# Optimization experiments

Measured on AMD Instinct MI355X. Metric: run time of the kernel, lower is better.

Reference implementation:

```python
import jax, jax.numpy as jnp
import numpy as np

NUM_EXPERTS = 8
TOP_K = 2


def setup_inputs() -> dict:
    key = jax.random.key(0)
    ks = jax.random.split(key, 5)
    B, S, D, F, E = 4, 2048, 1024, 4096, NUM_EXPERTS
    scale = 0.02
    x = jax.random.normal(ks[0], (B, S, D), dtype=jnp.float32)
    W_gate = jax.random.normal(ks[1], (E, D), dtype=jnp.float32) * scale  # router: logits = x @ W_gate.T
    Wg = jax.random.normal(ks[2], (E, F, D), dtype=jnp.float32) * scale   # per-expert gate_proj
    Wu = jax.random.normal(ks[3], (E, F, D), dtype=jnp.float32) * scale   # per-expert up_proj
    Wd = jax.random.normal(ks[4], (E, D, F), dtype=jnp.float32) * scale   # per-expert down_proj
    return {"x": x, "W_gate": W_gate, "Wg": Wg, "Wu": Wu, "Wd": Wd}


def reference(x, W_gate, Wg, Wu, Wd):
    # Router: softmax over experts, then top-k, renormalize.
    gate_logits = jnp.einsum('bsd,ed->bse', x, W_gate)
    probs = jax.nn.softmax(gate_logits, axis=-1)
    top_w, top_i = jax.lax.top_k(probs, TOP_K)                # (B,S,K)
    top_w = top_w / jnp.sum(top_w, axis=-1, keepdims=True)

    output = jnp.zeros_like(x)
    for e in range(NUM_EXPERTS):
        # combined routing weight for expert e (0 for tokens not routed to e)
        w_e = jnp.sum(jnp.where(top_i == e, top_w, 0.0), axis=-1)  # (B,S)
        gate = jax.nn.silu(jnp.einsum('bsd,fd->bsf', x, Wg[e]))
        up = jnp.einsum('bsd,fd->bsf', x, Wu[e])
        out_e = jnp.einsum('bsf,df->bsd', gate * up, Wd[e])
        output = output + out_e * w_e[..., None]
    return output
```

## Files before the change

### kernel.cpp

```cpp
#include <hip/hip_runtime.h>
#include <hip/hip_bf16.h>

#define T_TOK 8192
#define D_DIM 1024
#define F_DIM 4096
#define NE 8

#define BM 128
#define BK 32

#define BM2 256
#define BN2 128
#define BK2 64
#define KT2 (D_DIM / BK2)

typedef _Float16 v8h __attribute__((ext_vector_type(8)));
typedef float f32x4 __attribute__((ext_vector_type(4)));

__device__ __forceinline__ void async_lds16(void* lds, const void* g) {
    __builtin_amdgcn_global_load_lds(
        (const __attribute__((address_space(1))) void*)g,
        (__attribute__((address_space(3))) void*)lds,
        16, 0, 0);
}

template<int OFF>
__device__ __forceinline__ v8h ds128(unsigned a) {
    v8h r;
    asm volatile("ds_read_b128 %0, %1 offset:%2" : "=v"(r) : "v"(a), "n"(OFF));
    return r;
}

#define LGKM0 asm volatile("s_waitcnt lgkmcnt(0)" ::: "memory")
#define VMCNT0 asm volatile("s_waitcnt vmcnt(0)" ::: "memory")
#define SB0 __builtin_amdgcn_sched_barrier(0)

__global__ void router_kernel(const float* __restrict__ x,
                              const float* __restrict__ Wgate,
                              int* __restrict__ cnt,
                              int* __restrict__ rows,
                              float* __restrict__ wts) {
    int t = blockIdx.x;
    int lane = threadIdx.x;
    const float* xr = x + (size_t)t * D_DIM;
    float acc[NE];
#pragma unroll
    for (int e = 0; e < NE; ++e) acc[e] = 0.f;
#pragma unroll
    for (int i = 0; i < D_DIM / 64; ++i) {
        int d = i * 64 + lane;
        float xv = xr[d];
#pragma unroll
        for (int e = 0; e < NE; ++e) acc[e] += xv * Wgate[e * D_DIM + d];
    }
#pragma unroll
    for (int off = 32; off > 0; off >>= 1) {
#pragma unroll
        for (int e = 0; e < NE; ++e) acc[e] += __shfl_xor(acc[e], off, 64);
    }
    if (lane == 0) {
        int e0 = 0;
#pragma unroll
        for (int e = 1; e < NE; ++e) if (acc[e] > acc[e0]) e0 = e;
        int e1 = (e0 == 0) ? 1 : 0;
#pragma unroll
        for (int e = 0; e < NE; ++e) if (e != e0 && acc[e] > acc[e1]) e1 = e;
        float w0 = 1.f / (1.f + __expf(acc[e1] - acc[e0]));
        float w1 = 1.f - w0;
        int p0 = atomicAdd(&cnt[e0], 1);
        rows[e0 * T_TOK + p0] = 2 * t;
        wts[e0 * T_TOK + p0] = w0;
        int p1 = atomicAdd(&cnt[e1], 1);
        rows[e1 * T_TOK + p1] = 2 * t + 1;
        wts[e1 * T_TOK + p1] = w1;
    }
}

__global__ void f32to16_kernel(const float* __restrict__ src, _Float16* __restrict__ dst) {
    int i = blockIdx.x * blockDim.x + threadIdx.x;
    float4 v = ((const float4*)src)[i];
    union { _Float16 h[4]; uint2 u; } pk;
    pk.h[0] = (_Float16)v.x; pk.h[1] = (_Float16)v.y;
    pk.h[2] = (_Float16)v.z; pk.h[3] = (_Float16)v.w;
    *(uint2*)&dst[(size_t)i * 4] = pk.u;
}

__global__ __launch_bounds__(512, 2)
void gateup_kernel(const _Float16* __restrict__ Xh,
                   const _Float16* __restrict__ Wgh,
                   const _Float16* __restrict__ Wuh,
                   const int* __restrict__ cnt,
                   const int* __restrict__ rows,
                   const float* __restrict__ wts,
                   _Float16* __restrict__ H) {
    int e = blockIdx.z;
    int c = cnt[e];
    int row0 = blockIdx.y * BM2;
    if (row0 >= c) return;
    int col0 = blockIdx.x * BN2;

    __shared__ __align__(16) _Float16 Ab[2][BM2][BK2];
    __shared__ __align__(16) _Float16 Bb[2][BM2][BK2];
    __shared__ int hrow_s[BM2];
    __shared__ float w_s[BM2];

    int tid = threadIdx.x;
    int lane = tid & 63;
    int wv = tid >> 6;
    int wr = wv >> 2;
    int wc = wv & 3;

    if (tid < BM2) {
        int p = row0 + tid;
        if (p < c) { hrow_s[tid] = rows[e * T_TOK + p]; w_s[tid] = wts[e * T_TOK + p]; }
        else       { hrow_s[tid] = -1;                  w_s[tid] = 0.f; }
    }
    __syncthreads();

    int l8 = lane >> 3;
    int g  = lane & 7;
    int lg = g ^ l8;

    int r0 = wv * 16 + l8;
    int r1 = r0 + 8;

    int hA00 = hrow_s[r0],       hA01 = hrow_s[r1];
    int hA10 = hrow_s[128 + r0], hA11 = hrow_s[128 + r1];
    const _Float16* sA00 = Xh + (size_t)(hA00 >= 0 ? (hA00 >> 1) : 0) * D_DIM + lg * 8;
    const _Float16* sA01 = Xh + (size_t)(hA01 >= 0 ? (hA01 >> 1) : 0) * D_DIM + lg * 8;
    const _Float16* sA10 = Xh + (size_t)(hA10 >= 0 ? (hA10 >> 1) : 0) * D_DIM + lg * 8;
    const _Float16* sA11 = Xh + (size_t)(hA11 >= 0 ? (hA11 >> 1) : 0) * D_DIM + lg * 8;
    const _Float16* sB00 = Wgh + ((size_t)e * F_DIM + col0 + r0) * D_DIM + lg * 8;
    const _Float16* sB01 = Wgh + ((size_t)e * F_DIM + col0 + r1) * D_DIM + lg * 8;
    const _Float16* sB10 = Wuh + ((size_t)e * F_DIM + col0 + r0) * D_DIM + lg * 8;
    const _Float16* sB11 = Wuh + ((size_t)e * F_DIM + col0 + r1) * D_DIM + lg * 8;

    int stO0 = wv * 2048 + lane * 16;

    int m16 = lane & 15, q4 = lane >> 4;
    int rx = m16 & 7;
    int cb0 = ((q4 ^ rx) << 4);
    int cb1 = (((4 + q4) ^ rx) << 4);

    unsigned Abase = (unsigned)(size_t)(__attribute__((address_space(3))) void*)&Ab[0][0][0]
                     + (unsigned)((wr * 16 + m16) * 128);
    unsigned Bbase = (unsigned)(size_t)(__attribute__((address_space(3))) void*)&Bb[0][0][0]
                     + (unsigned)(m16 * 128 + wc * 4096);
    unsigned A0 = Abase + cb0, A1 = Abase + cb1;
    unsigned B0 = Bbase + cb0, B1 = Bbase + cb1;

    {
        char* a0 = (char*)Ab + stO0;
        char* b0 = (char*)Bb + stO0;
        async_lds16(b0,                sB00);
        async_lds16(b0 + 1024,         sB01);
        async_lds16(a0,                sA00);
        async_lds16(a0 + 1024,         sA01);
        async_lds16(b0 + 16384,        sB10);
        async_lds16(b0 + 16384 + 1024, sB11);
        async_lds16(a0 + 16384,        sA10);
        async_lds16(a0 + 16384 + 1024, sA11);
    }

    f32x4 accg[8][2], accu[8][2];
#pragma unroll
    for (int i = 0; i < 8; ++i)
#pragma unroll
        for (int j = 0; j < 2; ++j) { accg[i][j] = (f32x4)0.f; accu[i][j] = (f32x4)0.f; }

    int cur = 0;
#pragma unroll 1
    for (int t = 0; t < KT2; ++t) {
        int kn = (t + 1 < KT2) ? (t + 1) * BK2 : 0;
        int nb = cur ^ 1;

        VMCNT0;
        __builtin_amdgcn_s_barrier();
        SB0;

        {
            char* aD = (char*)Ab + nb * 32768 + stO0;
            char* bD = (char*)Bb + nb * 32768 + stO0;
            async_lds16(bD,                sB00 + kn);
            async_lds16(bD + 1024,         sB01 + kn);
            async_lds16(aD,                sA00 + kn);
            async_lds16(aD + 1024,         sA01 + kn);
            async_lds16(bD + 16384,        sB10 + kn);
            async_lds16(bD + 16384 + 1024, sB11 + kn);
            async_lds16(aD + 16384,        sA10 + kn);
            async_lds16(aD + 16384 + 1024, sA11 + kn);
        }
        SB0;

        unsigned cOff = (unsigned)(cur * 32768);
        unsigned a0 = A0 + cOff, a1 = A1 + cOff;
        unsigned b0 = B0 + cOff, b1 = B1 + cOff;

        v8h af[4][2], bg[2][2], bu[2][2];

        af[0][0] = ds128<0>(a0);      af[0][1] = ds128<0>(a1);
        af[1][0] = ds128<4096>(a0);   af[1][1] = ds128<4096>(a1);
        af[2][0] = ds128<8192>(a0);   af[2][1] = ds128<8192>(a1);
        af[3][0] = ds128<12288>(a0);  af[3][1] = ds128<12288>(a1);
        bg[0][0] = ds128<0>(b0);      bg[0][1] = ds128<0>(b1);
        bg[1][0] = ds128<2048>(b0);   bg[1][1] = ds128<2048>(b1);
        bu[0][0] = ds128<16384>(b0);  bu[0][1] = ds128<16384>(b1);
        bu[1][0] = ds128<18432>(b0);  bu[1][1] = ds128<18432>(b1);
        LGKM0;
        SB0;

        __builtin_amdgcn_s_setprio(1);
#pragma unroll
        for (int i = 0; i < 4; ++i)
#pragma unroll
            for (int j = 0; j < 2; ++j) {
                accg[i][j] = __builtin_amdgcn_mfma_f32_16x16x32_f16(af[i][0], bg[j][0], accg[i][j], 0, 0, 0);
                accg[i][j] = __builtin_amdgcn_mfma_f32_16x16x32_f16(af[i][1], bg[j][1], accg[i][j], 0, 0, 0);
            }
#pragma unroll
        for (int i = 0; i < 4; ++i)
#pragma unroll
            for (int j = 0; j < 2; ++j) {
                accu[i][j] = __builtin_amdgcn_mfma_f32_16x16x32_f16(af[i][0], bu[j][0], accu[i][j], 0, 0, 0);
                accu[i][j] = __builtin_amdgcn_mfma_f32_16x16x32_f16(af[i][1], bu[j][1], accu[i][j], 0, 0, 0);
            }
        __builtin_amdgcn_s_setprio(0);
        SB0;

        af[0][0] = ds128<16384>(a0);  af[0][1] = ds128<16384>(a1);
        af[1][0] = ds128<20480>(a0);  af[1][1] = ds128<20480>(a1);
        af[2][0] = ds128<24576>(a0);  af[2][1] = ds128<24576>(a1);
        af[3][0] = ds128<28672>(a0);  af[3][1] = ds128<28672>(a1);
        LGKM0;
        SB0;

        __builtin_amdgcn_s_setprio(1);
#pragma unroll
        for (int i = 0; i < 4; ++i)
#pragma unroll
            for (int j = 0; j < 2; ++j) {
                accg[i + 4][j] = __builtin_amdgcn_mfma_f32_16x16x32_f16(af[i][0], bg[j][0], accg[i + 4][j], 0, 0, 0);
                accg[i + 4][j] = __builtin_amdgcn_mfma_f32_16x16x32_f16(af[i][1], bg[j][1], accg[i + 4][j], 0, 0, 0);
            }
#pragma unroll
        for (int i = 0; i < 4; ++i)
#pragma unroll
            for (int j = 0; j < 2; ++j) {
                accu[i + 4][j] = __builtin_amdgcn_mfma_f32_16x16x32_f16(af[i][0], bu[j][0], accu[i + 4][j], 0, 0, 0);
                accu[i + 4][j] = __builtin_amdgcn_mfma_f32_16x16x32_f16(af[i][1], bu[j][1], accu[i + 4][j], 0, 0, 0);
            }
        __builtin_amdgcn_s_setprio(0);

        cur = nb;
    }

    int cl = lane & 15;
#pragma unroll
    for (int i = 0; i < 8; ++i) {
#pragma unroll
        for (int j = 0; j < 2; ++j) {
            f32x4 gv = accg[i][j];
            f32x4 uv = accu[i][j];
#pragma unroll
            for (int r4 = 0; r4 < 4; ++r4) {
                int r = i * 32 + wr * 16 + q4 * 4 + r4;
                int hr = hrow_s[r];
                if (hr < 0) continue;
                float gg = gv[r4];
                float h = gg / (1.f + __expf(-gg)) * w_s[r] * uv[r4];
                H[(size_t)hr * F_DIM + col0 + (wc * 2 + j) * 16 + cl] = (_Float16)h;
            }
        }
    }
}

__global__ __launch_bounds__(256, 2)
void down_kernel(const _Float16* __restrict__ H,
                 const _Float16* __restrict__ Wdh,
                 const int* __restrict__ cnt,
                 const int* __restrict__ rows,
                 float* __restrict__ O) {
    int e = blockIdx.z;
    int c = cnt[e];
    int row0 = blockIdx.y * BM;
    if (row0 >= c) return;
    int col0 = blockIdx.x * 128;

    __shared__ __align__(16) _Float16 As[BM][BK];
    __shared__ __align__(16) _Float16 Bs[128][BK];
    __shared__ int hrow_s[BM];

    int tid = threadIdx.x;
    int lane = tid & 63;
    int wave = tid >> 6;
    int wr = wave >> 1, wc = wave & 1;

    if (tid < BM) {
        int p = row0 + tid;
        hrow_s[tid] = (p < c) ? rows[e * T_TOK + p] : -1;
    }
    __syncthreads();

    int srow = tid >> 2;
    int kch = tid & 3;
    int hr0 = hrow_s[srow], hr1 = hrow_s[srow + 64];
    int r0 = (hr0 >= 0) ? hr0 : 0;
    int r1 = (hr1 >= 0) ? hr1 : 0;

    const _Float16* a0 = H + (size_t)r0 * F_DIM + kch * 8;
    const _Float16* a1 = H + (size_t)r1 * F_DIM + kch * 8;
    const _Float16* b0 = Wdh + ((size_t)e * D_DIM + col0 + srow) * F_DIM + kch * 8;
    const _Float16* b1 = b0 + (size_t)64 * F_DIM;

    _Float16* lA0 = &As[srow][kch * 8];
    _Float16* lA1 = &As[srow + 64][kch * 8];
    _Float16* lB0 = &Bs[srow][kch * 8];
    _Float16* lB1 = &Bs[srow + 64][kch * 8];

    f32x4 acc[4][4];
#pragma unroll
    for (int i = 0; i < 4; ++i)
#pragma unroll
        for (int j = 0; j < 4; ++j) acc[i][j] = (f32x4)0.f;

    int m16 = lane & 15, q8 = (lane >> 4) * 8;

    for (int k0 = 0; k0 < F_DIM; k0 += BK) {
        async_lds16(lA0, a0 + k0);
        async_lds16(lA1, a1 + k0);
        async_lds16(lB0, b0 + k0);
        async_lds16(lB1, b1 + k0);
        __syncthreads();

        v8h af[4], bf[4];
#pragma unroll
        for (int i = 0; i < 4; ++i)
            af[i] = *(const v8h*)&As[wr * 64 + i * 16 + m16][q8];
#pragma unroll
        for (int j = 0; j < 4; ++j)
            bf[j] = *(const v8h*)&Bs[wc * 64 + j * 16 + m16][q8];
#pragma unroll
        for (int i = 0; i < 4; ++i)
#pragma unroll
            for (int j = 0; j < 4; ++j)
                acc[i][j] = __builtin_amdgcn_mfma_f32_16x16x32_f16(af[i], bf[j], acc[i][j], 0, 0, 0);
        __syncthreads();
    }

    int q = lane >> 4, cl = lane & 15;
#pragma unroll
    for (int i = 0; i < 4; ++i) {
#pragma unroll
        for (int r4 = 0; r4 < 4; ++r4) {
            int r = wr * 64 + i * 16 + q * 4 + r4;
            int hr = hrow_s[r];
            if (hr < 0) continue;
#pragma unroll
            for (int j = 0; j < 4; ++j) {
                int col = col0 + wc * 64 + j * 16 + cl;
                O[(size_t)hr * D_DIM + col] = acc[i][j][r4];
            }
        }
    }
}

__global__ void combine_kernel(const float* __restrict__ O, float* __restrict__ out) {
    int t = blockIdx.x;
    int d = threadIdx.x;
    const float4* a = (const float4*)(O + (size_t)(2 * t) * D_DIM);
    const float4* b = (const float4*)(O + (size_t)(2 * t + 1) * D_DIM);
    float4 va = a[d], vb = b[d];
    float4 r; r.x = va.x + vb.x; r.y = va.y + vb.y; r.z = va.z + vb.z; r.w = va.w + vb.w;
    ((float4*)(out + (size_t)t * D_DIM))[d] = r;
}

extern "C" void kernel_launch(void* const* d_in, const int* in_sizes, int n_in,
                              void* d_out, int out_size, void* d_ws, size_t ws_size,
                              hipStream_t stream) {
    const float* x     = (const float*)d_in[0];
    const float* Wgate = (const float*)d_in[1];
    const float* Wg    = (const float*)d_in[2];
    const float* Wu    = (const float*)d_in[3];
    const float* Wd    = (const float*)d_in[4];
    float* out = (float*)d_out;

    char* w = (char*)d_ws;
    int*      cnt  = (int*)w;
    int*      rows = (int*)(w + 1024);
    float*    wts  = (float*)(w + 263168);
    _Float16* Xh   = (_Float16*)(w + 525312);

    const size_t OFF_WGH = 17302528;
    const size_t OFF_WUH = 84411392;
    const size_t OFF_WDH = 151520256;
    const size_t OFF_H   = 218629120;
    const size_t OFF_O   = 352846848;

    _Float16* Wgh = (_Float16*)(w + OFF_WGH);
    _Float16* Wuh = (_Float16*)(w + OFF_WUH);
    _Float16* Wdh = (_Float16*)(w + OFF_WDH);
    _Float16* H   = (_Float16*)(w + OFF_H);
    float*    O   = (float*)(w + OFF_O);

    hipMemsetAsync(w, 0, 1024, stream);

    router_kernel<<<T_TOK, 64, 0, stream>>>(x, Wgate, cnt, rows, wts);
    f32to16_kernel<<<(T_TOK * D_DIM / 4) / 256, 256, 0, stream>>>(x, Xh);

    const int WN4 = (NE * F_DIM * D_DIM / 4);
    f32to16_kernel<<<WN4 / 256, 256, 0, stream>>>(Wg, Wgh);
    f32to16_kernel<<<WN4 / 256, 256, 0, stream>>>(Wu, Wuh);
    f32to16_kernel<<<WN4 / 256, 256, 0, stream>>>(Wd, Wdh);

    gateup_kernel<<<dim3(F_DIM / BN2, T_TOK / BM2, NE), 512, 0, stream>>>(
        Xh, Wgh, Wuh, cnt, rows, wts, H);
    down_kernel<<<dim3(D_DIM / 128, T_TOK / BM, NE), 256, 0, stream>>>(
        H, Wdh, cnt, rows, O);
    combine_kernel<<<T_TOK, 256, 0, stream>>>(O, out);
}
```

Baseline: 1.183 ms.

## Double-buffer down-projection GEMM with swizzled LDS and larger 256x128 tiles

Rewrites the down-projection kernel to use 256-row tiles with 512 threads, a BK of 64, and double-buffered LDS filled by async global-to-LDS loads so the next tile's fetch overlaps the current tile's MFMAs. LDS layout is XOR-swizzled and read with explicit ds_read_b128, and wave priority is raised around the MFMA block. The goal is to hide memory latency, cut barriers per K step, and increase reuse of the expert weight tile. Larger tiles waste more work on partially filled expert row blocks, and LDS use grows, which can limit occupancy.

```diff
diff --git a/kernel.cpp b/kernel.cpp
--- a/kernel.cpp
+++ b/kernel.cpp
@@ -6,13 +6,11 @@
 #define F_DIM 4096
 #define NE 8
 
-#define BM 128
-#define BK 32
-
 #define BM2 256
 #define BN2 128
 #define BK2 64
 #define KT2 (D_DIM / BK2)
+#define KTD (F_DIM / BK2)
 
 typedef _Float16 v8h __attribute__((ext_vector_type(8)));
 typedef float f32x4 __attribute__((ext_vector_type(4)));
@@ -274,7 +272,7 @@
     }
 }
 
-__global__ __launch_bounds__(256, 2)
+__global__ __launch_bounds__(512, 2)
 void down_kernel(const _Float16* __restrict__ H,
                  const _Float16* __restrict__ Wdh,
                  const int* __restrict__ cnt,
@@ -282,40 +280,66 @@
                  float* __restrict__ O) {
     int e = blockIdx.z;
     int c = cnt[e];
-    int row0 = blockIdx.y * BM;
+    int row0 = blockIdx.y * BM2;
     if (row0 >= c) return;
     int col0 = blockIdx.x * 128;
 
-    __shared__ __align__(16) _Float16 As[BM][BK];
-    __shared__ __align__(16) _Float16 Bs[128][BK];
-    __shared__ int hrow_s[BM];
+    __shared__ __align__(16) _Float16 Ab[2][BM2][BK2];
+    __shared__ __align__(16) _Float16 Bb[2][128][BK2];
+    __shared__ int hrow_s[BM2];
 
     int tid = threadIdx.x;
     int lane = tid & 63;
-    int wave = tid >> 6;
-    int wr = wave >> 1, wc = wave & 1;
-
-    if (tid < BM) {
+    int wv = tid >> 6;
+    int wr = wv >> 1;
+    int wc = wv & 1;
+
+    if (tid < BM2) {
         int p = row0 + tid;
         hrow_s[tid] = (p < c) ? rows[e * T_TOK + p] : -1;
     }
     __syncthreads();
 
-    int srow = tid >> 2;
-    int kch = tid & 3;
-    int hr0 = hrow_s[srow], hr1 = hrow_s[srow + 64];
-    int r0 = (hr0 >= 0) ? hr0 : 0;
-    int r1 = (hr1 >= 0) ? hr1 : 0;
-
-    const _Float16* a0 = H + (size_t)r0 * F_DIM + kch * 8;
-    const _Float16* a1 = H + (size_t)r1 * F_DIM + kch * 8;
-    const _Float16* b0 = Wdh + ((size_t)e * D_DIM + col0 + srow) * F_DIM + kch * 8;
-    const _Float16* b1 = b0 + (size_t)64 * F_DIM;
-
-    _Float16* lA0 = &As[srow][kch * 8];
-    _Float16* lA1 = &As[srow + 64][kch * 8];
-    _Float16* lB0 = &Bs[srow][kch * 8];
-    _Float16* lB1 = &Bs[srow + 64][kch * 8];
+    int l8 = lane >> 3;
+    int g  = lane & 7;
+    int lg = g ^ l8;
+
+    int r0 = wv * 16 + l8;
+    int r1 = r0 + 8;
+
+    int hA00 = hrow_s[r0],       hA01 = hrow_s[r1];
+    int hA10 = hrow_s[128 + r0], hA11 = hrow_s[128 + r1];
+    const _Float16* sA00 = H + (size_t)(hA00 >= 0 ? hA00 : 0) * F_DIM + lg * 8;
+    const _Float16* sA01 = H + (size_t)(hA01 >= 0 ? hA01 : 0) * F_DIM + lg * 8;
+    const _Float16* sA10 = H + (size_t)(hA10 >= 0 ? hA10 : 0) * F_DIM + lg * 8;
+    const _Float16* sA11 = H + (size_t)(hA11 >= 0 ? hA11 : 0) * F_DIM + lg * 8;
+    const _Float16* sB00 = Wdh + ((size_t)e * D_DIM + col0 + r0) * F_DIM + lg * 8;
+    const _Float16* sB01 = Wdh + ((size_t)e * D_DIM + col0 + r1) * F_DIM + lg * 8;
+
+    int stO0 = wv * 2048 + lane * 16;
+
+    int m16 = lane & 15, q4 = lane >> 4;
+    int rx = m16 & 7;
+    int cb0 = ((q4 ^ rx) << 4);
+    int cb1 = (((4 + q4) ^ rx) << 4);
+
+    unsigned Abase = (unsigned)(size_t)(__attribute__((address_space(3))) void*)&Ab[0][0][0]
+                     + (unsigned)((wr * 64 + m16) * 128);
+    unsigned Bbase = (unsigned)(size_t)(__attribute__((address_space(3))) void*)&Bb[0][0][0]
+                     + (unsigned)((wc * 64 + m16) * 128);
+    unsigned A0 = Abase + cb0, A1 = Abase + cb1;
+    unsigned B0 = Bbase + cb0, B1 = Bbase + cb1;
+
+    {
+        char* a0 = (char*)Ab + stO0;
+        char* b0 = (char*)Bb + stO0;
+        async_lds16(b0,                sB00);
+        async_lds16(b0 + 1024,         sB01);
+        async_lds16(a0,                sA00);
+        async_lds16(a0 + 1024,         sA01);
+        async_lds16(a0 + 16384,        sA10);
+        async_lds16(a0 + 16384 + 1024, sA11);
+    }
 
     f32x4 acc[4][4];
 #pragma unroll
@@ -323,36 +347,65 @@
 #pragma unroll
         for (int j = 0; j < 4; ++j) acc[i][j] = (f32x4)0.f;
 
-    int m16 = lane & 15, q8 = (lane >> 4) * 8;
-
-    for (int k0 = 0; k0 < F_DIM; k0 += BK) {
-        async_lds16(lA0, a0 + k0);
-        async_lds16(lA1, a1 + k0);
-        async_lds16(lB0, b0 + k0);
-        async_lds16(lB1, b1 + k0);
-        __syncthreads();
-
-        v8h af[4], bf[4];
+    int cur = 0;
+#pragma unroll 1
+    for (int t = 0; t < KTD; ++t) {
+        int kn = (t + 1 < KTD) ? (t + 1) * BK2 : 0;
+        int nb = cur ^ 1;
+
+        VMCNT0;
+        __builtin_amdgcn_s_barrier();
+        SB0;
+
+        {
+            char* aD = (char*)Ab + nb * 32768 + stO0;
+            char* bD = (char*)Bb + nb * 16384 + stO0;
+            async_lds16(bD,                sB00 + kn);
+            async_lds16(bD + 1024,         sB01 + kn);
+            async_lds16(aD,                sA00 + kn);
+            async_lds16(aD + 1024,         sA01 + kn);
+            async_lds16(aD + 16384,        sA10 + kn);
+            async_lds16(aD + 16384 + 1024, sA11 + kn);
+        }
+        SB0;
+
+        unsigned a0 = A0 + (unsigned)(cur * 32768);
+        unsigned a1 = A1 + (unsigned)(cur * 32768);
+        unsigned b0 = B0 + (unsigned)(cur * 16384);
+        unsigned b1 = B1 + (unsigned)(cur * 16384);
+
+        v8h af[4][2], bf[4][2];
+
+        af[0][0] = ds128<0>(a0);      af[0][1] = ds128<0>(a1);
+        af[1][0] = ds128<2048>(a0);   af[1][1] = ds128<2048>(a1);
+        af[2][0] = ds128<4096>(a0);   af[2][1] = ds128<4096>(a1);
+        af[3][0] = ds128<6144>(a0);   af[3][1] = ds128<6144>(a1);
+        bf[0][0] = ds128<0>(b0);      bf[0][1] = ds128<0>(b1);
+        bf[1][0] = ds128<2048>(b0);   bf[1][1] = ds128<2048>(b1);
+        bf[2][0] = ds128<4096>(b0);   bf[2][1] = ds128<4096>(b1);
+        bf[3][0] = ds128<6144>(b0);   bf[3][1] = ds128<6144>(b1);
+        LGKM0;
+        SB0;
+
+        __builtin_amdgcn_s_setprio(1);
 #pragma unroll
         for (int i = 0; i < 4; ++i)
-            af[i] = *(const v8h*)&As[wr * 64 + i * 16 + m16][q8];
-#pragma unroll
-        for (int j = 0; j < 4; ++j)
-            bf[j] = *(const v8h*)&Bs[wc * 64 + j * 16 + m16][q8];
-#pragma unroll
-        for (int i = 0; i < 4; ++i)
-#pragma unroll
-            for (int j = 0; j < 4; ++j)
-                acc[i][j] = __builtin_amdgcn_mfma_f32_16x16x32_f16(af[i], bf[j], acc[i][j], 0, 0, 0);
-        __syncthreads();
-    }
-
-    int q = lane >> 4, cl = lane & 15;
+#pragma unroll
+            for (int j = 0; j < 4; ++j) {
+                acc[i][j] = __builtin_amdgcn_mfma_f32_16x16x32_f16(af[i][0], bf[j][0], acc[i][j], 0, 0, 0);
+                acc[i][j] = __builtin_amdgcn_mfma_f32_16x16x32_f16(af[i][1], bf[j][1], acc[i][j], 0, 0, 0);
+            }
+        __builtin_amdgcn_s_setprio(0);
+
+        cur = nb;
+    }
+
+    int cl = lane & 15;
 #pragma unroll
     for (int i = 0; i < 4; ++i) {
 #pragma unroll
         for (int r4 = 0; r4 < 4; ++r4) {
-            int r = wr * 64 + i * 16 + q * 4 + r4;
+            int r = wr * 64 + i * 16 + q4 * 4 + r4;
             int hr = hrow_s[r];
             if (hr < 0) continue;
 #pragma unroll
@@ -414,7 +467,7 @@
 
     gateup_kernel<<<dim3(F_DIM / BN2, T_TOK / BM2, NE), 512, 0, stream>>>(
         Xh, Wgh, Wuh, cnt, rows, wts, H);
-    down_kernel<<<dim3(D_DIM / 128, T_TOK / BM, NE), 256, 0, stream>>>(
+    down_kernel<<<dim3(D_DIM / 128, T_TOK / BM2, NE), 512, 0, stream>>>(
         H, Wdh, cnt, rows, O);
     combine_kernel<<<T_TOK, 256, 0, stream>>>(O, out);
 }
```

Result: no change. 1.180 ms (-0.3%).
